# Kernel tuning notes

Hardware: AMD Instinct MI355X
Metric: run time of the kernel (lower is better)

## Reference

```python
import jax, jax.numpy as jnp
import numpy as np

B, S, D = 4, 2048, 512
DT_RANK, N = 32, 16  # dt_rank, d_state
EPS = 1e-5


def setup_inputs() -> dict:
    key = jax.random.key(0)
    ks = jax.random.split(key, 8)
    def w(k, shape, scale):
        return jax.random.normal(k, shape, dtype=jnp.float32) * scale
    return {
        "x": w(ks[0], (B, S, D), 1.0),
        "gamma": jnp.ones((D,), jnp.float32),
        "beta": jnp.zeros((D,), jnp.float32),
        "W_proj": w(ks[1], (D, D), D ** -0.5),
        "b_proj": jnp.zeros((D,), jnp.float32),
        "W_fwd": w(ks[2], (D, D), D ** -0.5),
        "b_fwd": jnp.zeros((D,), jnp.float32),
        "W_bwd": w(ks[3], (D, D), D ** -0.5),
        "b_bwd": jnp.zeros((D,), jnp.float32),
        "W_dbc": w(ks[4], (D, DT_RANK + 2 * N), D ** -0.5),
        "W_dt": w(ks[5], (DT_RANK, D), DT_RANK ** -0.5),
        "b_dt": jnp.zeros((D,), jnp.float32),
        "A_log": jnp.log(jnp.tile(jnp.arange(1, N + 1, dtype=jnp.float32), (D, 1))),
        "D_ssm": jnp.ones((D,), jnp.float32),
    }


def _ssm(x, A_log, D_ssm, W_dbc, W_dt, b_dt):
    # x: (B, S, D) with D == dim_inner
    A = -jnp.exp(A_log)                                   # (D, N)
    dbc = x @ W_dbc                                       # (B, S, dt_rank + 2N)
    delta = jax.nn.softplus(dbc[..., :DT_RANK] @ W_dt + b_dt)  # (B, S, D)
    Bm = dbc[..., DT_RANK:DT_RANK + N]                    # (B, S, N)
    Cm = dbc[..., DT_RANK + N:]                           # (B, S, N)
    deltaA = jnp.exp(delta[..., None] * A)                # (B, S, D, N)
    BX = (delta * x)[..., None] * Bm[:, :, None, :]       # (B, S, D, N)
    def combine(c1, c2):
        a1, b1 = c1
        a2, b2 = c2
        return a1 * a2, a2 * b1 + b2
    _, hs = jax.lax.associative_scan(combine, (deltaA, BX), axis=1)
    y = jnp.einsum('bsdn,bsn->bsd', hs, Cm) + D_ssm * x
    return y


def reference(x, gamma, beta, W_proj, b_proj, W_fwd, b_fwd, W_bwd, b_bwd,
              W_dbc, W_dt, b_dt, A_log, D_ssm):
    skip = x
    mu = jnp.mean(x, axis=-1, keepdims=True)
    var = jnp.var(x, axis=-1, keepdims=True)
    xn = (x - mu) * jax.lax.rsqrt(var + EPS) * gamma + beta
    z1 = xn @ W_proj + b_proj
    x1 = z1  # source applies the SAME self.proj twice -> identical outputs
    # kernel-size-1 conv1d == pointwise linear over channels
    fwd = x1 @ W_fwd + b_fwd
    x1_ssm = _ssm(fwd, A_log, D_ssm, W_dbc, W_dt, b_dt)  # computed but unused in source (dead code)
    bwd = x1 @ W_bwd + bb if False else x1 @ W_bwd + b_bwd
    x2 = _ssm(bwd, A_log, D_ssm, W_dbc, W_dt, b_dt)
    z = jax.nn.silu(z1)
    return x1 * z + x2 * z + skip
```

## Files before the change

### kernel.cpp

```cpp
#include <hip/hip_runtime.h>
#include <hip/hip_bf16.h>
#include <math.h>

#define Bb 4
#define Sdim 2048
#define Ddim 512
#define Nn16 16
#define TOK 8192
#define NCh 64
#define LCh 32

using bf16x8 = __attribute__((ext_vector_type(8))) __bf16;
using f32x4  = __attribute__((ext_vector_type(4))) float;

__device__ __forceinline__ unsigned short f2bf(float f) {
    unsigned int u = __float_as_uint(f);
    u += 0x7fffu + ((u >> 16) & 1u);
    return (unsigned short)(u >> 16);
}
__device__ __forceinline__ float bf2f(unsigned short h) {
    return __uint_as_float(((unsigned int)h) << 16);
}

#define GLD16(g, l) __builtin_amdgcn_global_load_lds( \
    (const __attribute__((address_space(1))) void*)(g), \
    (__attribute__((address_space(3))) void*)(l), 16, 0, 0)

__device__ __forceinline__ float softplus_f(float v) {
    return v > 20.f ? v : log1pf(__expf(v));
}

__global__ __launch_bounds__(256) void prep_all(
    const float* __restrict__ x, const float* __restrict__ gamma, const float* __restrict__ beta,
    const float* __restrict__ Wp, const float* __restrict__ Wb,
    const float* __restrict__ Wdbc, const float* __restrict__ Wdt,
    ushort* __restrict__ xn, ushort* __restrict__ Wpt, ushort* __restrict__ Wbt,
    ushort* __restrict__ Wdbct, ushort* __restrict__ WdtT)
{
    int blk = blockIdx.x;
    int tid = threadIdx.x;
    if (blk < 560) {
        __shared__ float tb[32 * 33];
        int xx = tid & 31, yy0 = tid >> 5;
        const float* in; ushort* outT; int K, N, bx, by;
        if (blk < 256)      { in = Wp;   outT = Wpt;   K = 512; N = 512; bx = (blk & 15) * 32; by = (blk >> 4) * 32; }
        else if (blk < 512) { int t = blk - 256; in = Wb; outT = Wbt; K = 512; N = 512; bx = (t & 15) * 32; by = (t >> 4) * 32; }
        else if (blk < 544) { int t = blk - 512; in = Wdbc; outT = Wdbct; K = 512; N = 64; bx = (t & 1) * 32; by = (t >> 1) * 32; }
        else                { int t = blk - 544; in = Wdt; outT = WdtT; K = 32; N = 512; bx = t * 32; by = 0; }
        #pragma unroll
        for (int yy = yy0; yy < 32; yy += 8)
            tb[yy * 33 + xx] = in[(size_t)(by + yy) * N + bx + xx];
        __syncthreads();
        #pragma unroll
        for (int yy = yy0; yy < 32; yy += 8)
            outT[(size_t)(bx + yy) * K + by + xx] = f2bf(tb[xx * 33 + yy]);
    } else {
        int bid = blk - 560;
        int w = tid >> 6, lane = tid & 63;
        const float4* g4 = (const float4*)gamma;
        const float4* b4 = (const float4*)beta;
        float4 g0 = g4[lane], g1 = g4[lane + 64];
        float4 be0 = b4[lane], be1 = b4[lane + 64];
        for (int rr = 0; rr < 8; ++rr) {
            int row = bid * 32 + w * 8 + rr;
            const float4* xr = (const float4*)(x + (size_t)row * Ddim);
            float4 v0 = xr[lane];
            float4 v1 = xr[lane + 64];
            float s = v0.x + v0.y + v0.z + v0.w + v1.x + v1.y + v1.z + v1.w;
            float q = v0.x*v0.x + v0.y*v0.y + v0.z*v0.z + v0.w*v0.w
                    + v1.x*v1.x + v1.y*v1.y + v1.z*v1.z + v1.w*v1.w;
            #pragma unroll
            for (int m = 1; m <= 32; m <<= 1) { s += __shfl_xor(s, m); q += __shfl_xor(q, m); }
            float mu = s * (1.0f / Ddim);
            float var = q * (1.0f / Ddim) - mu * mu;
            float rs = rsqrtf(var + 1e-5f);
            ushort4 u0, u1;
            u0.x = f2bf((v0.x - mu) * rs * g0.x + be0.x);
            u0.y = f2bf((v0.y - mu) * rs * g0.y + be0.y);
            u0.z = f2bf((v0.z - mu) * rs * g0.z + be0.z);
            u0.w = f2bf((v0.w - mu) * rs * g0.w + be0.w);
            u1.x = f2bf((v1.x - mu) * rs * g1.x + be1.x);
            u1.y = f2bf((v1.y - mu) * rs * g1.y + be1.y);
            u1.z = f2bf((v1.z - mu) * rs * g1.z + be1.z);
            u1.w = f2bf((v1.w - mu) * rs * g1.w + be1.w);
            *(ushort4*)(xn + (size_t)row * Ddim + lane * 4) = u0;
            *(ushort4*)(xn + (size_t)row * Ddim + 256 + lane * 4) = u1;
        }
    }
}

__global__ __launch_bounds__(256) void gemm_bf(
    const ushort* __restrict__ A,
    const ushort* __restrict__ Bt,
    const float* __restrict__ bias,
    ushort* __restrict__ Cb)
{
    __shared__ __align__(16) ushort As[128 * 32];
    __shared__ __align__(16) ushort Bs[128 * 32];
    int tid = threadIdx.x, w = tid >> 6, lane = tid & 63;
    int bm = blockIdx.y * 128, bn = blockIdx.x * 128;
    int wm = (w & 1) * 64, wn = (w >> 1) * 64;
    int quad = lane >> 4, l16 = lane & 15;
    int srow = lane >> 2, schunk = (lane & 3) * 8;
    f32x4 acc[4][4] = {};

    for (int k0 = 0; k0 < 512; k0 += 32) {
        __syncthreads();
        #pragma unroll
        for (int s = 0; s < 2; ++s) {
            int r = w * 32 + s * 16;
            GLD16(A  + (size_t)(bm + r + srow) * 512 + k0 + schunk, &As[r * 32]);
            GLD16(Bt + (size_t)(bn + r + srow) * 512 + k0 + schunk, &Bs[r * 32]);
        }
        __syncthreads();
        bf16x8 af[4], bfr[4];
        #pragma unroll
        for (int i = 0; i < 4; ++i)
            af[i] = *(const bf16x8*)(const void*)&As[(wm + 16 * i + l16) * 32 + quad * 8];
        #pragma unroll
        for (int j = 0; j < 4; ++j)
            bfr[j] = *(const bf16x8*)(const void*)&Bs[(wn + 16 * j + l16) * 32 + quad * 8];
        #pragma unroll
        for (int i = 0; i < 4; ++i)
            #pragma unroll
            for (int j = 0; j < 4; ++j)
                acc[i][j] = __builtin_amdgcn_mfma_f32_16x16x32_bf16(af[i], bfr[j], acc[i][j], 0, 0, 0);
    }
    #pragma unroll
    for (int i = 0; i < 4; ++i) {
        int row = bm + wm + 16 * i + quad * 4;
        #pragma unroll
        for (int j = 0; j < 4; ++j) {
            int col = bn + wn + 16 * j + l16;
            float bv = bias[col];
            #pragma unroll
            for (int r = 0; r < 4; ++r)
                Cb[(size_t)(row + r) * 512 + col] = f2bf(acc[i][j][r] + bv);
        }
    }
}

__global__ __launch_bounds__(256) void gemm_dbc(
    const ushort* __restrict__ A,
    const ushort* __restrict__ Bt,
    ushort* __restrict__ dbc,
    float* __restrict__ BC)
{
    __shared__ __align__(16) ushort As[128 * 32];
    __shared__ __align__(16) ushort Bs[64 * 32];
    int tid = threadIdx.x, w = tid >> 6, lane = tid & 63;
    int bm = blockIdx.y * 128;
    int wm = w * 32;
    int quad = lane >> 4, l16 = lane & 15;
    int srow = lane >> 2, schunk = (lane & 3) * 8;
    f32x4 acc[2][4] = {};

    for (int k0 = 0; k0 < 512; k0 += 32) {
        __syncthreads();
        #pragma unroll
        for (int s = 0; s < 2; ++s) {
            int r = w * 32 + s * 16;
            GLD16(A + (size_t)(bm + r + srow) * 512 + k0 + schunk, &As[r * 32]);
        }
        {
            int r = w * 16;
            GLD16(Bt + (size_t)(r + srow) * 512 + k0 + schunk, &Bs[r * 32]);
        }
        __syncthreads();
        bf16x8 af[2], bfr[4];
        #pragma unroll
        for (int i = 0; i < 2; ++i)
            af[i] = *(const bf16x8*)(const void*)&As[(wm + 16 * i + l16) * 32 + quad * 8];
        #pragma unroll
        for (int j = 0; j < 4; ++j)
            bfr[j] = *(const bf16x8*)(const void*)&Bs[(16 * j + l16) * 32 + quad * 8];
        #pragma unroll
        for (int i = 0; i < 2; ++i)
            #pragma unroll
            for (int j = 0; j < 4; ++j)
                acc[i][j] = __builtin_amdgcn_mfma_f32_16x16x32_bf16(af[i], bfr[j], acc[i][j], 0, 0, 0);
    }
    #pragma unroll
    for (int i = 0; i < 2; ++i) {
        int row = bm + wm + 16 * i + quad * 4;
        #pragma unroll
        for (int j = 0; j < 4; ++j) {
            int col = 16 * j + l16;
            #pragma unroll
            for (int r = 0; r < 4; ++r) {
                float v = acc[i][j][r];
                if (col < 32) dbc[(size_t)(row + r) * 32 + col] = f2bf(v);
                else          BC [(size_t)(row + r) * 32 + col - 32] = v;
            }
        }
    }
}

__global__ __launch_bounds__(256) void gemm_delta(
    const ushort* __restrict__ A, const ushort* __restrict__ Bt,
    const float* __restrict__ b_dt, ushort* __restrict__ delta)
{
    __shared__ __align__(16) ushort As[128 * 32];
    __shared__ __align__(16) ushort Bs[128 * 32];
    int tid = threadIdx.x, w = tid >> 6, lane = tid & 63;
    int bm = blockIdx.y * 128, bn = blockIdx.x * 128;
    int wm = (w & 1) * 64, wn = (w >> 1) * 64;
    int quad = lane >> 4, l16 = lane & 15;
    int srow16 = lane >> 2, sch = (lane & 3) * 8;

    #pragma unroll
    for (int s = 0; s < 2; ++s) {
        int r = w * 32 + s * 16;
        GLD16(A  + (size_t)(bm + r + srow16) * 32 + sch, &As[r * 32]);
        GLD16(Bt + (size_t)(bn + r + srow16) * 32 + sch, &Bs[r * 32]);
    }
    __syncthreads();
    bf16x8 af[4], bfr[4];
    #pragma unroll
    for (int i = 0; i < 4; ++i)
        af[i] = *(const bf16x8*)(const void*)&As[(wm + 16 * i + l16) * 32 + quad * 8];
    #pragma unroll
    for (int j = 0; j < 4; ++j)
        bfr[j] = *(const bf16x8*)(const void*)&Bs[(wn + 16 * j + l16) * 32 + quad * 8];
    f32x4 acc[4][4] = {};
    #pragma unroll
    for (int i = 0; i < 4; ++i)
        #pragma unroll
        for (int j = 0; j < 4; ++j)
            acc[i][j] = __builtin_amdgcn_mfma_f32_16x16x32_bf16(af[i], bfr[j], acc[i][j], 0, 0, 0);
    #pragma unroll
    for (int i = 0; i < 4; ++i) {
        int row = bm + wm + 16 * i + quad * 4;
        #pragma unroll
        for (int j = 0; j < 4; ++j) {
            int col = bn + wn + 16 * j + l16;
            float bv = b_dt[col];
            #pragma unroll
            for (int r = 0; r < 4; ++r)
                delta[(size_t)(row + r) * 512 + col] = f2bf(softplus_f(acc[i][j][r] + bv));
        }
    }
}

__global__ __launch_bounds__(256) void scan_pass1(
    const ushort* __restrict__ delta, const ushort* __restrict__ bwd,
    const float* __restrict__ BC, const float* __restrict__ A_log,
    float* __restrict__ hend, float* __restrict__ sdbuf)
{
    int d = (blockIdx.x << 8) + threadIdx.x;
    int c = blockIdx.y;
    int b = blockIdx.z;

    float A[16];
    {
        const float4* al = (const float4*)(A_log + (size_t)d * 16);
        #pragma unroll
        for (int i = 0; i < 4; ++i) {
            float4 v = al[i];
            A[4*i+0] = -__expf(v.x); A[4*i+1] = -__expf(v.y);
            A[4*i+2] = -__expf(v.z); A[4*i+3] = -__expf(v.w);
        }
    }
    float h[16];
    #pragma unroll
    for (int n = 0; n < 16; ++n) h[n] = 0.f;
    float sd = 0.f;

    size_t base = ((size_t)(b * Sdim + c * LCh)) * Ddim + d;
    const float* bcrow = BC + ((size_t)(b * Sdim + c * LCh)) * 32;

    #pragma unroll 2
    for (int i = 0; i < LCh; ++i) {
        float dlt = bf2f(delta[base + (size_t)i * Ddim]);
        float bw  = bf2f(bwd [base + (size_t)i * Ddim]);
        float4 B0 = *(const float4*)(bcrow + i * 32 + 0);
        float4 B1 = *(const float4*)(bcrow + i * 32 + 4);
        float4 B2 = *(const float4*)(bcrow + i * 32 + 8);
        float4 B3 = *(const float4*)(bcrow + i * 32 + 12);
        sd += dlt;
        float xb = dlt * bw;
        float Bv[16] = {B0.x,B0.y,B0.z,B0.w, B1.x,B1.y,B1.z,B1.w,
                        B2.x,B2.y,B2.z,B2.w, B3.x,B3.y,B3.z,B3.w};
        #pragma unroll
        for (int n = 0; n < 16; ++n)
            h[n] = fmaf(__expf(dlt * A[n]), h[n], xb * Bv[n]);
    }
    size_t cidx = ((((size_t)b * NCh + c) * Ddim) + d) * 16;
    float4* ho = (float4*)(hend + cidx);
    ho[0] = make_float4(h[0],  h[1],  h[2],  h[3]);
    ho[1] = make_float4(h[4],  h[5],  h[6],  h[7]);
    ho[2] = make_float4(h[8],  h[9],  h[10], h[11]);
    ho[3] = make_float4(h[12], h[13], h[14], h[15]);
    sdbuf[((size_t)b * NCh + c) * Ddim + d] = sd;
}

__global__ __launch_bounds__(256) void scan_pass2(
    float* __restrict__ hend, const float* __restrict__ sdbuf,
    const float* __restrict__ A_log)
{
    int gl = blockIdx.x * 256 + threadIdx.x;
    int b = gl >> 13;
    int r = gl & 8191;
    int d = r >> 4;
    float A = -__expf(A_log[r]);
    float hin = 0.f;
    for (int c0 = 0; c0 < NCh; c0 += 8) {
        float he[8], dec[8];
        #pragma unroll
        for (int u = 0; u < 8; ++u) {
            size_t idx = (((size_t)b * NCh + c0 + u) * Ddim) * 16 + r;
            he[u]  = hend[idx];
            dec[u] = __expf(A * sdbuf[((size_t)b * NCh + c0 + u) * Ddim + d]);
        }
        #pragma unroll
        for (int u = 0; u < 8; ++u) {
            size_t idx = (((size_t)b * NCh + c0 + u) * Ddim) * 16 + r;
            hend[idx] = hin;
            hin = fmaf(dec[u], hin, he[u]);
        }
    }
}

__global__ __launch_bounds__(256) void scan_pass3(
    const ushort* __restrict__ delta, const ushort* __restrict__ bwd,
    const float* __restrict__ BC, const ushort* __restrict__ z1,
    const float* __restrict__ x, const float* __restrict__ A_log,
    const float* __restrict__ D_ssm, const float* __restrict__ hin,
    float* __restrict__ out)
{
    int d = (blockIdx.x << 8) + threadIdx.x;
    int c = blockIdx.y;
    int b = blockIdx.z;

    float A[16];
    {
        const float4* al = (const float4*)(A_log + (size_t)d * 16);
        #pragma unroll
        for (int i = 0; i < 4; ++i) {
            float4 v = al[i];
            A[4*i+0] = -__expf(v.x); A[4*i+1] = -__expf(v.y);
            A[4*i+2] = -__expf(v.z); A[4*i+3] = -__expf(v.w);
        }
    }
    float h[16];
    {
        size_t cidx = ((((size_t)b * NCh + c) * Ddim) + d) * 16;
        const float4* hi = (const float4*)(hin + cidx);
        float4 h0 = hi[0], h1 = hi[1], h2 = hi[2], h3 = hi[3];
        h[0]=h0.x; h[1]=h0.y; h[2]=h0.z; h[3]=h0.w;
        h[4]=h1.x; h[5]=h1.y; h[6]=h1.z; h[7]=h1.w;
        h[8]=h2.x; h[9]=h2.y; h[10]=h2.z; h[11]=h2.w;
        h[12]=h3.x; h[13]=h3.y; h[14]=h3.z; h[15]=h3.w;
    }
    float Dd = D_ssm[d];

    size_t base = ((size_t)(b * Sdim + c * LCh)) * Ddim + d;
    const float* bcrow = BC + ((size_t)(b * Sdim + c * LCh)) * 32;

    #pragma unroll 2
    for (int i = 0; i < LCh; ++i) {
        float dlt = bf2f(delta[base + (size_t)i * Ddim]);
        float bw  = bf2f(bwd [base + (size_t)i * Ddim]);
        float z1v = bf2f(z1  [base + (size_t)i * Ddim]);
        float xv  = x[base + (size_t)i * Ddim];
        float4 B0 = *(const float4*)(bcrow + i * 32 + 0);
        float4 B1 = *(const float4*)(bcrow + i * 32 + 4);
        float4 B2 = *(const float4*)(bcrow + i * 32 + 8);
        float4 B3 = *(const float4*)(bcrow + i * 32 + 12);
        float4 C0 = *(const float4*)(bcrow + i * 32 + 16);
        float4 C1 = *(const float4*)(bcrow + i * 32 + 20);
        float4 C2 = *(const float4*)(bcrow + i * 32 + 24);
        float4 C3 = *(const float4*)(bcrow + i * 32 + 28);
        float Bv[16] = {B0.x,B0.y,B0.z,B0.w, B1.x,B1.y,B1.z,B1.w,
                        B2.x,B2.y,B2.z,B2.w, B3.x,B3.y,B3.z,B3.w};
        float Cv[16] = {C0.x,C0.y,C0.z,C0.w, C1.x,C1.y,C1.z,C1.w,
                        C2.x,C2.y,C2.z,C2.w, C3.x,C3.y,C3.z,C3.w};
        float xb = dlt * bw;
        float y  = Dd * bw;
        #pragma unroll
        for (int n = 0; n < 16; ++n) {
            h[n] = fmaf(__expf(dlt * A[n]), h[n], xb * Bv[n]);
            y = fmaf(h[n], Cv[n], y);
        }
        float silu = z1v / (1.f + __expf(-z1v));
        out[base + (size_t)i * Ddim] = fmaf(z1v + y, silu, xv);
    }
}

extern "C" void kernel_launch(void* const* d_in, const int* in_sizes, int n_in,
                              void* d_out, int out_size, void* d_ws, size_t ws_size,
                              hipStream_t stream) {
    const float* x      = (const float*)d_in[0];
    const float* gamma  = (const float*)d_in[1];
    const float* beta   = (const float*)d_in[2];
    const float* W_proj = (const float*)d_in[3];
    const float* b_proj = (const float*)d_in[4];
    const float* W_bwd  = (const float*)d_in[7];
    const float* b_bwd  = (const float*)d_in[8];
    const float* W_dbc  = (const float*)d_in[9];
    const float* W_dt   = (const float*)d_in[10];
    const float* b_dt   = (const float*)d_in[11];
    const float* A_log  = (const float*)d_in[12];
    const float* D_ssm  = (const float*)d_in[13];
    float* out = (float*)d_out;

    char* p = (char*)d_ws;
    ushort* xn_bf    = (ushort*)p;
    ushort* z1_bf    = (ushort*)(p + (8ull  << 20));
    ushort* bwd_bf   = (ushort*)(p + (16ull << 20));
    ushort* delta_bf = (ushort*)(p + (24ull << 20));
    ushort* dbc_bf   = (ushort*)(p + (32ull << 20));
    float*  BC       = (float*) (p + (33ull << 20));
    float*  hend     = (float*) (p + (34ull << 20));
    float*  sdbuf    = (float*) (p + (42ull << 20));
    ushort* Wpt      = (ushort*)(p + (43ull << 20));
    ushort* Wbt      = Wpt   + (size_t)512 * 512;
    ushort* Wdbct    = Wbt   + (size_t)512 * 512;
    ushort* WdtT     = Wdbct + (size_t)64 * 512;

    prep_all<<<dim3(816), dim3(256), 0, stream>>>(
        x, gamma, beta, W_proj, W_bwd, W_dbc, W_dt, xn_bf, Wpt, Wbt, Wdbct, WdtT);
    gemm_bf<<<dim3(4, 64), dim3(256), 0, stream>>>(xn_bf, Wpt, b_proj, z1_bf);
    gemm_bf<<<dim3(4, 64), dim3(256), 0, stream>>>(z1_bf, Wbt, b_bwd, bwd_bf);
    gemm_dbc<<<dim3(1, 64), dim3(256), 0, stream>>>(bwd_bf, Wdbct, dbc_bf, BC);
    gemm_delta<<<dim3(4, 64), dim3(256), 0, stream>>>(dbc_bf, WdtT, b_dt, delta_bf);
    scan_pass1<<<dim3(2, NCh, Bb), dim3(256), 0, stream>>>(delta_bf, bwd_bf, BC, A_log, hend, sdbuf);
    scan_pass2<<<dim3(128), dim3(256), 0, stream>>>(hend, sdbuf, A_log);
    scan_pass3<<<dim3(2, NCh, Bb), dim3(256), 0, stream>>>(delta_bf, bwd_bf, BC, z1_bf, x, A_log, D_ssm, hend, out);
}
```

Measured before the change: 206.0 us.

## Retile GEMMs to 64x64 with swizzled LDS and fuse dbc and delta projections

The main projection GEMMs move from 128x128 tiles with K-step 32 to 64x64 tiles with K-step 64, which launches 1024 blocks instead of 256 for more parallelism across CUs. They also use an XOR-swizzled LDS layout to cut bank conflicts. The dbc and delta GEMMs become a single kernel that keeps the dt-rank slice in shared memory, which removes the dbc round trip through global memory and one launch. In exchange, the smaller tiles give less data reuse per block, and the fused kernel handles only 32 rows per block.

```diff
diff --git a/kernel.cpp b/kernel.cpp
--- a/kernel.cpp
+++ b/kernel.cpp
@@ -89,155 +89,140 @@
     }
 }
 
-__global__ __launch_bounds__(256) void gemm_bf(
+__global__ __launch_bounds__(256) void gemm64(
     const ushort* __restrict__ A,
     const ushort* __restrict__ Bt,
     const float* __restrict__ bias,
     ushort* __restrict__ Cb)
 {
-    __shared__ __align__(16) ushort As[128 * 32];
-    __shared__ __align__(16) ushort Bs[128 * 32];
+    __shared__ __align__(16) ushort As[64 * 64];
+    __shared__ __align__(16) ushort Bs[64 * 64];
     int tid = threadIdx.x, w = tid >> 6, lane = tid & 63;
-    int bm = blockIdx.y * 128, bn = blockIdx.x * 128;
-    int wm = (w & 1) * 64, wn = (w >> 1) * 64;
+    int bm = blockIdx.x * 64, bn = blockIdx.y * 64;
     int quad = lane >> 4, l16 = lane & 15;
-    int srow = lane >> 2, schunk = (lane & 3) * 8;
-    f32x4 acc[4][4] = {};
-
-    for (int k0 = 0; k0 < 512; k0 += 32) {
+    int srow8 = lane >> 3;
+    int scolx = ((lane & 7) ^ srow8) * 8;
+    int cof0 = (quad ^ (l16 & 7)) * 8;
+    int cof1 = ((4 + quad) ^ (l16 & 7)) * 8;
+    f32x4 acc[4] = {};
+
+    for (int k0 = 0; k0 < 512; k0 += 64) {
+        __syncthreads();
+        #pragma unroll
+        for (int s = 0; s < 2; ++s) {
+            int r = w * 16 + s * 8;
+            GLD16(A  + (size_t)(bm + r + srow8) * 512 + k0 + scolx, &As[r * 64]);
+            GLD16(Bt + (size_t)(bn + r + srow8) * 512 + k0 + scolx, &Bs[r * 64]);
+        }
+        __syncthreads();
+        #pragma unroll
+        for (int ks = 0; ks < 2; ++ks) {
+            int cof = ks ? cof1 : cof0;
+            bf16x8 bfr = *(const bf16x8*)(const void*)&Bs[(w * 16 + l16) * 64 + cof];
+            #pragma unroll
+            for (int i = 0; i < 4; ++i) {
+                bf16x8 af = *(const bf16x8*)(const void*)&As[(16 * i + l16) * 64 + cof];
+                acc[i] = __builtin_amdgcn_mfma_f32_16x16x32_bf16(af, bfr, acc[i], 0, 0, 0);
+            }
+        }
+    }
+    int col = bn + w * 16 + l16;
+    float bv = bias[col];
+    #pragma unroll
+    for (int i = 0; i < 4; ++i) {
+        int row = bm + 16 * i + quad * 4;
+        #pragma unroll
+        for (int r = 0; r < 4; ++r)
+            Cb[(size_t)(row + r) * 512 + col] = f2bf(acc[i][r] + bv);
+    }
+}
+
+__global__ __launch_bounds__(256) void dbc_delta(
+    const ushort* __restrict__ bwd,
+    const ushort* __restrict__ Wdbct,
+    const ushort* __restrict__ WdtT,
+    const float* __restrict__ b_dt,
+    float* __restrict__ BC,
+    ushort* __restrict__ delta)
+{
+    __shared__ __align__(16) ushort As[32 * 64];
+    __shared__ __align__(16) ushort Bs[64 * 64];
+    __shared__ __align__(16) ushort sdbc[32 * 32];
+    int tid = threadIdx.x, w = tid >> 6, lane = tid & 63;
+    int bm = blockIdx.x * 32;
+    int quad = lane >> 4, l16 = lane & 15;
+    int srow8 = lane >> 3;
+    int scolx = ((lane & 7) ^ srow8) * 8;
+    int cof0 = (quad ^ (l16 & 7)) * 8;
+    int cof1 = ((4 + quad) ^ (l16 & 7)) * 8;
+
+    f32x4 acc[2] = {};
+    for (int k0 = 0; k0 < 512; k0 += 64) {
+        __syncthreads();
+        {
+            int r = w * 8;
+            GLD16(bwd + (size_t)(bm + r + srow8) * 512 + k0 + scolx, &As[r * 64]);
+        }
+        #pragma unroll
+        for (int s = 0; s < 2; ++s) {
+            int r = w * 16 + s * 8;
+            GLD16(Wdbct + (size_t)(r + srow8) * 512 + k0 + scolx, &Bs[r * 64]);
+        }
+        __syncthreads();
+        #pragma unroll
+        for (int ks = 0; ks < 2; ++ks) {
+            int cof = ks ? cof1 : cof0;
+            bf16x8 bfr = *(const bf16x8*)(const void*)&Bs[(w * 16 + l16) * 64 + cof];
+            #pragma unroll
+            for (int i = 0; i < 2; ++i) {
+                bf16x8 af = *(const bf16x8*)(const void*)&As[(16 * i + l16) * 64 + cof];
+                acc[i] = __builtin_amdgcn_mfma_f32_16x16x32_bf16(af, bfr, acc[i], 0, 0, 0);
+            }
+        }
+    }
+    {
+        int col = w * 16 + l16;
+        #pragma unroll
+        for (int i = 0; i < 2; ++i) {
+            int rl = 16 * i + quad * 4;
+            #pragma unroll
+            for (int r = 0; r < 4; ++r) {
+                float v = acc[i][r];
+                if (col < 32) sdbc[(rl + r) * 32 + col] = f2bf(v);
+                else          BC[(size_t)(bm + rl + r) * 32 + col - 32] = v;
+            }
+        }
+    }
+    __syncthreads();
+    bf16x8 af2[2];
+    #pragma unroll
+    for (int i = 0; i < 2; ++i)
+        af2[i] = *(const bf16x8*)(const void*)&sdbc[(16 * i + l16) * 32 + quad * 8];
+    int srow16 = lane >> 2, sch = (lane & 3) * 8;
+    for (int cn = 0; cn < 4; ++cn) {
         __syncthreads();
         #pragma unroll
         for (int s = 0; s < 2; ++s) {
             int r = w * 32 + s * 16;
-            GLD16(A  + (size_t)(bm + r + srow) * 512 + k0 + schunk, &As[r * 32]);
-            GLD16(Bt + (size_t)(bn + r + srow) * 512 + k0 + schunk, &Bs[r * 32]);
-        }
-        __syncthreads();
-        bf16x8 af[4], bfr[4];
-        #pragma unroll
-        for (int i = 0; i < 4; ++i)
-            af[i] = *(const bf16x8*)(const void*)&As[(wm + 16 * i + l16) * 32 + quad * 8];
-        #pragma unroll
-        for (int j = 0; j < 4; ++j)
-            bfr[j] = *(const bf16x8*)(const void*)&Bs[(wn + 16 * j + l16) * 32 + quad * 8];
-        #pragma unroll
-        for (int i = 0; i < 4; ++i)
-            #pragma unroll
-            for (int j = 0; j < 4; ++j)
-                acc[i][j] = __builtin_amdgcn_mfma_f32_16x16x32_bf16(af[i], bfr[j], acc[i][j], 0, 0, 0);
-    }
-    #pragma unroll
-    for (int i = 0; i < 4; ++i) {
-        int row = bm + wm + 16 * i + quad * 4;
-        #pragma unroll
-        for (int j = 0; j < 4; ++j) {
-            int col = bn + wn + 16 * j + l16;
-            float bv = bias[col];
-            #pragma unroll
-            for (int r = 0; r < 4; ++r)
-                Cb[(size_t)(row + r) * 512 + col] = f2bf(acc[i][j][r] + bv);
-        }
-    }
-}
-
-__global__ __launch_bounds__(256) void gemm_dbc(
-    const ushort* __restrict__ A,
-    const ushort* __restrict__ Bt,
-    ushort* __restrict__ dbc,
-    float* __restrict__ BC)
-{
-    __shared__ __align__(16) ushort As[128 * 32];
-    __shared__ __align__(16) ushort Bs[64 * 32];
-    int tid = threadIdx.x, w = tid >> 6, lane = tid & 63;
-    int bm = blockIdx.y * 128;
-    int wm = w * 32;
-    int quad = lane >> 4, l16 = lane & 15;
-    int srow = lane >> 2, schunk = (lane & 3) * 8;
-    f32x4 acc[2][4] = {};
-
-    for (int k0 = 0; k0 < 512; k0 += 32) {
-        __syncthreads();
-        #pragma unroll
-        for (int s = 0; s < 2; ++s) {
-            int r = w * 32 + s * 16;
-            GLD16(A + (size_t)(bm + r + srow) * 512 + k0 + schunk, &As[r * 32]);
-        }
-        {
-            int r = w * 16;
-            GLD16(Bt + (size_t)(r + srow) * 512 + k0 + schunk, &Bs[r * 32]);
-        }
-        __syncthreads();
-        bf16x8 af[2], bfr[4];
-        #pragma unroll
-        for (int i = 0; i < 2; ++i)
-            af[i] = *(const bf16x8*)(const void*)&As[(wm + 16 * i + l16) * 32 + quad * 8];
-        #pragma unroll
-        for (int j = 0; j < 4; ++j)
-            bfr[j] = *(const bf16x8*)(const void*)&Bs[(16 * j + l16) * 32 + quad * 8];
-        #pragma unroll
-        for (int i = 0; i < 2; ++i)
-            #pragma unroll
-            for (int j = 0; j < 4; ++j)
-                acc[i][j] = __builtin_amdgcn_mfma_f32_16x16x32_bf16(af[i], bfr[j], acc[i][j], 0, 0, 0);
-    }
-    #pragma unroll
-    for (int i = 0; i < 2; ++i) {
-        int row = bm + wm + 16 * i + quad * 4;
-        #pragma unroll
-        for (int j = 0; j < 4; ++j) {
-            int col = 16 * j + l16;
-            #pragma unroll
-            for (int r = 0; r < 4; ++r) {
-                float v = acc[i][j][r];
-                if (col < 32) dbc[(size_t)(row + r) * 32 + col] = f2bf(v);
-                else          BC [(size_t)(row + r) * 32 + col - 32] = v;
+            GLD16(WdtT + (size_t)(cn * 128 + r + srow16) * 32 + sch, &Bs[r * 32]);
+        }
+        __syncthreads();
+        #pragma unroll
+        for (int j = 0; j < 2; ++j) {
+            bf16x8 bfr = *(const bf16x8*)(const void*)&Bs[(w * 32 + j * 16 + l16) * 32 + quad * 8];
+            f32x4 a2[2] = {};
+            #pragma unroll
+            for (int i = 0; i < 2; ++i)
+                a2[i] = __builtin_amdgcn_mfma_f32_16x16x32_bf16(af2[i], bfr, a2[i], 0, 0, 0);
+            int col = cn * 128 + w * 32 + j * 16 + l16;
+            float bv = b_dt[col];
+            #pragma unroll
+            for (int i = 0; i < 2; ++i) {
+                int row = bm + 16 * i + quad * 4;
+                #pragma unroll
+                for (int r = 0; r < 4; ++r)
+                    delta[(size_t)(row + r) * 512 + col] = f2bf(softplus_f(a2[i][r] + bv));
             }
-        }
-    }
-}
-
-__global__ __launch_bounds__(256) void gemm_delta(
-    const ushort* __restrict__ A, const ushort* __restrict__ Bt,
-    const float* __restrict__ b_dt, ushort* __restrict__ delta)
-{
-    __shared__ __align__(16) ushort As[128 * 32];
-    __shared__ __align__(16) ushort Bs[128 * 32];
-    int tid = threadIdx.x, w = tid >> 6, lane = tid & 63;
-    int bm = blockIdx.y * 128, bn = blockIdx.x * 128;
-    int wm = (w & 1) * 64, wn = (w >> 1) * 64;
-    int quad = lane >> 4, l16 = lane & 15;
-    int srow16 = lane >> 2, sch = (lane & 3) * 8;
-
-    #pragma unroll
-    for (int s = 0; s < 2; ++s) {
-        int r = w * 32 + s * 16;
-        GLD16(A  + (size_t)(bm + r + srow16) * 32 + sch, &As[r * 32]);
-        GLD16(Bt + (size_t)(bn + r + srow16) * 32 + sch, &Bs[r * 32]);
-    }
-    __syncthreads();
-    bf16x8 af[4], bfr[4];
-    #pragma unroll
-    for (int i = 0; i < 4; ++i)
-        af[i] = *(const bf16x8*)(const void*)&As[(wm + 16 * i + l16) * 32 + quad * 8];
-    #pragma unroll
-    for (int j = 0; j < 4; ++j)
-        bfr[j] = *(const bf16x8*)(const void*)&Bs[(wn + 16 * j + l16) * 32 + quad * 8];
-    f32x4 acc[4][4] = {};
-    #pragma unroll
-    for (int i = 0; i < 4; ++i)
-        #pragma unroll
-        for (int j = 0; j < 4; ++j)
-            acc[i][j] = __builtin_amdgcn_mfma_f32_16x16x32_bf16(af[i], bfr[j], acc[i][j], 0, 0, 0);
-    #pragma unroll
-    for (int i = 0; i < 4; ++i) {
-        int row = bm + wm + 16 * i + quad * 4;
-        #pragma unroll
-        for (int j = 0; j < 4; ++j) {
-            int col = bn + wn + 16 * j + l16;
-            float bv = b_dt[col];
-            #pragma unroll
-            for (int r = 0; r < 4; ++r)
-                delta[(size_t)(row + r) * 512 + col] = f2bf(softplus_f(acc[i][j][r] + bv));
         }
     }
 }
@@ -409,7 +394,6 @@
     ushort* z1_bf    = (ushort*)(p + (8ull  << 20));
     ushort* bwd_bf   = (ushort*)(p + (16ull << 20));
     ushort* delta_bf = (ushort*)(p + (24ull << 20));
-    ushort* dbc_bf   = (ushort*)(p + (32ull << 20));
     float*  BC       = (float*) (p + (33ull << 20));
     float*  hend     = (float*) (p + (34ull << 20));
     float*  sdbuf    = (float*) (p + (42ull << 20));
@@ -420,10 +404,9 @@
 
     prep_all<<<dim3(816), dim3(256), 0, stream>>>(
         x, gamma, beta, W_proj, W_bwd, W_dbc, W_dt, xn_bf, Wpt, Wbt, Wdbct, WdtT);
-    gemm_bf<<<dim3(4, 64), dim3(256), 0, stream>>>(xn_bf, Wpt, b_proj, z1_bf);
-    gemm_bf<<<dim3(4, 64), dim3(256), 0, stream>>>(z1_bf, Wbt, b_bwd, bwd_bf);
-    gemm_dbc<<<dim3(1, 64), dim3(256), 0, stream>>>(bwd_bf, Wdbct, dbc_bf, BC);
-    gemm_delta<<<dim3(4, 64), dim3(256), 0, stream>>>(dbc_bf, WdtT, b_dt, delta_bf);
+    gemm64<<<dim3(128, 8), dim3(256), 0, stream>>>(xn_bf, Wpt, b_proj, z1_bf);
+    gemm64<<<dim3(128, 8), dim3(256), 0, stream>>>(z1_bf, Wbt, b_bwd, bwd_bf);
+    dbc_delta<<<dim3(256), dim3(256), 0, stream>>>(bwd_bf, Wdbct, WdtT, b_dt, BC, delta_bf);
     scan_pass1<<<dim3(2, NCh, Bb), dim3(256), 0, stream>>>(delta_bf, bwd_bf, BC, A_log, hend, sdbuf);
     scan_pass2<<<dim3(128), dim3(256), 0, stream>>>(hend, sdbuf, A_log);
     scan_pass3<<<dim3(2, NCh, Bb), dim3(256), 0, stream>>>(delta_bf, bwd_bf, BC, z1_bf, x, A_log, D_ssm, hend, out);
```

New measurement: 191.9 us. -6.8%, faster.
